# Kernel tuning notes

Hardware: AMD Instinct MI355X
Metric: run time of the kernel (lower is better)

Reference implementation:

```python
import jax, jax.numpy as jnp
import numpy as np

B, T, D, H = 4, 2048, 512, 8
SCALE = np.float32(1.0 / np.sqrt(D))  # 'vaswani' scale, tied scalar, non-trainable
MASK_BIAS = np.float32(1e9)           # TF dense_attention masking constant


def setup_inputs() -> dict:
    key = jax.random.key(0)
    ks = jax.random.split(key, 5)
    s = 0.02  # small init so softmax logits are well-scaled
    return {
        "query": jax.random.normal(ks[0], (B, T, D), jnp.float32),
        "value": jax.random.normal(ks[1], (B, T, D), jnp.float32),
        "Wq": jax.random.normal(ks[2], (D, D * H), jnp.float32) * s,
        "bq": jnp.zeros((D * H,), jnp.float32),
        "Wk": jax.random.normal(ks[3], (D, D * H), jnp.float32) * s,
        "bk": jnp.zeros((D * H,), jnp.float32),
        "Wv": jax.random.normal(ks[4], (D, D * H), jnp.float32) * s,
        "bv": jnp.zeros((D * H,), jnp.float32),
    }


def reference(query, value, Wq, bq, Wk, bk, Wv, bv):
    # Per-head Dense projections (linear activation, depth=1): [B,T,D] -> [B,T,H*D]
    # split(axis=-1) into H heads + concat(axis=0) == reshape to [B,T,H,D]
    # (head h occupies contiguous slice [h*D:(h+1)*D] of the last axis)
    q = (query @ Wq + bq).reshape(B, T, H, D)
    k = (value @ Wk + bk).reshape(B, T, H, D)  # key defaults to value
    v = (value @ Wv + bv).reshape(B, T, H, D)
    # multiplicative scores: matmul(scale*q, k^T) -> [B,H,Tq,Tv]
    scores = jnp.einsum('bqhd,bkhd->bhqk', SCALE * q, k)
    # causal mask applied TF-style: scores -= 1e9 * (~mask)
    causal = jnp.tril(jnp.ones((T, T), bool))
    scores = jnp.where(causal, scores, scores - MASK_BIAS)
    attn = jax.nn.softmax(scores, axis=-1)          # [B,H,Tq,Tv]
    out = jnp.einsum('bhqk,bkhd->bqhd', attn, v)    # [B,Tq,H,D]
    # heads_output_mode='cat': concat heads back on feature axis
    return out.reshape(B, T, H * D)
```

## Files before the change

### kernel.cpp

```cpp
#include <hip/hip_runtime.h>
#include <stdint.h>

#define Bsz 4
#define Tsz 2048
#define Dsz 512
#define Hsz 8
#define HDsz 4096
#define Msz 8192
#define SCALE 0.044194173824159216f

typedef __attribute__((ext_vector_type(8))) short bf16x8;
typedef __attribute__((ext_vector_type(4))) float f32x4;
typedef __attribute__((ext_vector_type(4))) short s16x4;

static __device__ __forceinline__ short f2bf(float x) {
    uint32_t b = __float_as_uint(x);
    b += 0x7fff + ((b >> 16) & 1);
    return (short)(b >> 16);
}

__global__ __launch_bounds__(256) void xcast_kernel(
    const float* __restrict__ Xq, const float* __restrict__ Xv,
    short* __restrict__ Oq, short* __restrict__ Ov)
{
    int idx = blockIdx.x * 256 + threadIdx.x;
    const float* src = (idx < 1048576) ? Xq : Xv;
    short* dst = (idx < 1048576) ? Oq : Ov;
    int i = (idx < 1048576) ? idx : idx - 1048576;
    float4 v = *(const float4*)&src[(size_t)i * 4];
    s16x4 o;
    o.x = f2bf(v.x); o.y = f2bf(v.y); o.z = f2bf(v.z); o.w = f2bf(v.w);
    *(s16x4*)&dst[(size_t)i * 4] = o;
}

__global__ __launch_bounds__(256) void wtrans_kernel(
    const float* __restrict__ Wq, const float* __restrict__ Wk,
    const float* __restrict__ Wv, short* __restrict__ WtAll)
{
    const float* W = (blockIdx.z == 0) ? Wq : (blockIdx.z == 1) ? Wk : Wv;
    short* Wt = WtAll + (size_t)blockIdx.z * (size_t)HDsz * Dsz;
    __shared__ float tile[32][33];
    int tx = threadIdx.x, ty = threadIdx.y;
    int k0 = blockIdx.x * 32, n0 = blockIdx.y * 32;
    for (int i = 0; i < 4; i++)
        tile[ty + i * 8][tx] = W[(size_t)(k0 + ty + i * 8) * HDsz + n0 + tx];
    __syncthreads();
    for (int i = 0; i < 4; i++)
        Wt[(size_t)(n0 + ty + i * 8) * Dsz + k0 + tx] = f2bf(tile[tx][ty + i * 8]);
}

__global__ __launch_bounds__(256, 2) void proj_gemm_kernel(
    const short* __restrict__ Xqb, const short* __restrict__ Xvb,
    const short* __restrict__ WtAll, const float* __restrict__ bq,
    const float* __restrict__ bk, const float* __restrict__ bv,
    short* __restrict__ Qo, short* __restrict__ Ko, short* __restrict__ Vto)
{
    const int mode = blockIdx.z;
    const short* X = (mode == 0) ? Xqb : Xvb;
    const short* Wt = WtAll + (size_t)mode * (size_t)HDsz * Dsz;
    const float* bias = (mode == 0) ? bq : (mode == 1) ? bk : bv;
    const int m0 = blockIdx.x * 128, n0 = blockIdx.y * 128;

    __shared__ short sm[17408];

    const int tid = threadIdx.x;
    const int lane = tid & 63, wave = tid >> 6;
    const int quad = lane >> 4, l16 = lane & 15;
    const int wm = wave >> 1, wn = wave & 1;

    const int dmarow = lane >> 2;
    const int dmachunk = (lane & 3) ^ ((lane >> 3) & 3);
    const int rdsw = (quad ^ ((l16 >> 1) & 3)) * 8;

    f32x4 acc[4][4];
    for (int i = 0; i < 4; i++)
        for (int j = 0; j < 4; j++)
            acc[i][j] = f32x4{0.f, 0.f, 0.f, 0.f};

#define STAGE(ksv, bufsel) do {                                                  \
        const int _ks = (ksv);                                                   \
        short* _A = sm + (bufsel) * 4096;                                        \
        short* _B = sm + 8192 + (bufsel) * 4096;                                 \
        for (int s = 0; s < 2; s++) {                                            \
            int c = wave * 2 + s;                                                \
            int row = c * 16 + dmarow;                                           \
            const short* ga = X + (size_t)(m0 + row) * Dsz + _ks + dmachunk * 8; \
            __builtin_amdgcn_global_load_lds(                                    \
                (const __attribute__((address_space(1))) void*)ga,               \
                (__attribute__((address_space(3))) void*)&_A[c * 512], 16, 0, 0);\
            const short* gb = Wt + (size_t)(n0 + row) * Dsz + _ks + dmachunk * 8;\
            __builtin_amdgcn_global_load_lds(                                    \
                (const __attribute__((address_space(1))) void*)gb,               \
                (__attribute__((address_space(3))) void*)&_B[c * 512], 16, 0, 0);\
        }                                                                        \
    } while (0)

    STAGE(0, 0);
    __syncthreads();

    for (int t = 0; t < 16; t++) {
        const int cur = t & 1;
        if (t < 15) STAGE((t + 1) * 32, cur ^ 1);
        const short* Ac = sm + cur * 4096;
        const short* Bc = sm + 8192 + cur * 4096;
        bf16x8 af[4], bfr[4];
        for (int i = 0; i < 4; i++)
            af[i] = *(const bf16x8*)&Ac[(wm * 64 + i * 16 + l16) * 32 + rdsw];
        for (int j = 0; j < 4; j++)
            bfr[j] = *(const bf16x8*)&Bc[(wn * 64 + j * 16 + l16) * 32 + rdsw];
        for (int i = 0; i < 4; i++)
            for (int j = 0; j < 4; j++)
                acc[i][j] = __builtin_amdgcn_mfma_f32_16x16x32_bf16(
                    af[i], bfr[j], acc[i][j], 0, 0, 0);
        __syncthreads();
    }
#undef STAGE

    const int b = m0 >> 11, t0 = m0 & 2047;
    const int h = n0 >> 9, d0 = n0 & 511;
    const float scv = (mode == 0) ? SCALE : 1.0f;

    if (mode == 2) {
        for (int i = 0; i < 4; i++)
            for (int j = 0; j < 4; j++) {
                int c = wn * 64 + j * 16 + l16;
                float bb = bias[n0 + c];
                int rb = wm * 64 + i * 16 + quad * 4;
                for (int r = 0; r < 4; r++)
                    sm[c * 136 + rb + r] = f2bf(acc[i][j][r] + bb);
            }
    } else {
        for (int i = 0; i < 4; i++)
            for (int j = 0; j < 4; j++) {
                int c = wn * 64 + j * 16 + l16;
                float bb = bias[n0 + c];
                int rb = wm * 64 + i * 16 + quad * 4;
                for (int r = 0; r < 4; r++)
                    sm[(rb + r) * 136 + c] = f2bf((acc[i][j][r] + bb) * scv);
            }
    }
    __syncthreads();

    if (mode == 2) {
        size_t base = ((size_t)(b * Hsz + h) * Dsz + d0) * Tsz + t0;
        for (int k = 0; k < 8; k++) {
            int cid = k * 256 + tid;
            int c = cid >> 4, r8 = (cid & 15) * 8;
            *(bf16x8*)&Vto[base + (size_t)c * Tsz + r8] =
                *(const bf16x8*)&sm[c * 136 + r8];
        }
    } else {
        short* O = (mode == 0) ? Qo : Ko;
        size_t base = ((size_t)(b * Hsz + h) * Tsz + t0) * Dsz + d0;
        for (int k = 0; k < 8; k++) {
            int cid = k * 256 + tid;
            int r = cid >> 4, c8 = (cid & 15) * 8;
            *(bf16x8*)&O[base + (size_t)r * Dsz + c8] =
                *(const bf16x8*)&sm[r * 136 + c8];
        }
    }
}

__global__ __launch_bounds__(512, 2) void attn_kernel(
    const short* __restrict__ Q, const short* __restrict__ K,
    const short* __restrict__ Vt, float* __restrict__ out)
{
    extern __shared__ short smem[];

    const int bid = blockIdx.x;
    const int qt = 15 - (bid >> 5);
    const int bh = bid & 31;
    const int q0 = qt * 128;
    const short* Qb = Q + (size_t)bh * Tsz * Dsz;
    const short* Kb = K + (size_t)bh * Tsz * Dsz;
    const short* Vb = Vt + (size_t)bh * Dsz * Tsz;

    const int tid = threadIdx.x;
    const int lane = tid & 63, wave = tid >> 6;
    const int quad = lane >> 4, l16 = lane & 15;
    const int qw = q0 + wave * 16;
    short* Pw = smem + 74240 + wave * (16 * 40);
    const int vrow = tid >> 2, vch = tid & 3;

    bf16x8 qf[16];
    for (int ks = 0; ks < 16; ks++)
        qf[ks] = *(const bf16x8*)&Qb[(size_t)(qw + l16) * Dsz + ks * 32 + quad * 8];

    f32x4 acc[32];
    for (int dt = 0; dt < 32; dt++) acc[dt] = f32x4{0.f, 0.f, 0.f, 0.f};
    float lacc[4] = {0.f, 0.f, 0.f, 0.f};

    {
        short* Ks0 = smem;
        short* Vs0 = smem + 33280;
        for (int i = 0; i < 4; i++) {
            int r = wave * 4 + i;
            const short* gp = Kb + (size_t)r * Dsz + lane * 8;
            __builtin_amdgcn_global_load_lds(
                (const __attribute__((address_space(1))) void*)gp,
                (__attribute__((address_space(3))) void*)&Ks0[r * 520], 16, 0, 0);
        }
        for (int p = 0; p < 4; p++) {
            int row = p * 128 + vrow;
            bf16x8 v = *(const bf16x8*)&Vb[(size_t)row * Tsz + vch * 8];
            *(bf16x8*)&Vs0[row * 40 + vch * 8] = v;
        }
    }
    __syncthreads();

    const int nkv = 4 * (qt + 1);
    for (int kt = 0; kt < nkv; kt++) {
        const int kv0 = kt * 32;
        short* Ksc = smem + (kt & 1) * 16640;
        short* Vsc = smem + 33280 + (kt & 1) * 20480;
        const bool pref = (kt + 1 < nkv);

        bf16x8 vreg[4];
        if (pref) {
            const int kvn = kv0 + 32;
            short* Ksn = smem + ((kt + 1) & 1) * 16640;
            for (int i = 0; i < 4; i++) {
                int r = wave * 4 + i;
                const short* gp = Kb + (size_t)(kvn + r) * Dsz + lane * 8;
                __builtin_amdgcn_global_load_lds(
                    (const __attribute__((address_space(1))) void*)gp,
                    (__attribute__((address_space(3))) void*)&Ksn[r * 520], 16, 0, 0);
            }
            for (int p = 0; p < 4; p++) {
                int row = p * 128 + vrow;
                vreg[p] = *(const bf16x8*)&Vb[(size_t)row * Tsz + kvn + vch * 8];
            }
        }

        if (kv0 <= qw + 15) {
            f32x4 s0 = f32x4{0.f, 0.f, 0.f, 0.f}, s1 = f32x4{0.f, 0.f, 0.f, 0.f};
            for (int ks = 0; ks < 16; ks++) {
                bf16x8 b0 = *(const bf16x8*)&Ksc[l16 * 520 + ks * 32 + quad * 8];
                bf16x8 b1 = *(const bf16x8*)&Ksc[(16 + l16) * 520 + ks * 32 + quad * 8];
                s0 = __builtin_amdgcn_mfma_f32_16x16x32_bf16(qf[ks], b0, s0, 0, 0, 0);
                s1 = __builtin_amdgcn_mfma_f32_16x16x32_bf16(qf[ks], b1, s1, 0, 0, 0);
            }
            bool full = (kv0 + 31 <= qw);
            for (int r = 0; r < 4; r++) {
                int rowg = qw + quad * 4 + r;
                float p0 = __expf(fminf(s0[r], 40.f));
                float p1 = __expf(fminf(s1[r], 40.f));
                if (!full) {
                    if (kv0 + l16 > rowg) p0 = 0.f;
                    if (kv0 + 16 + l16 > rowg) p1 = 0.f;
                }
                lacc[r] += p0 + p1;
                Pw[(quad * 4 + r) * 40 + l16] = f2bf(p0);
                Pw[(quad * 4 + r) * 40 + 16 + l16] = f2bf(p1);
            }
            bf16x8 pa = *(const bf16x8*)&Pw[l16 * 40 + quad * 8];
            for (int dt = 0; dt < 32; dt++) {
                bf16x8 vb = *(const bf16x8*)&Vsc[(dt * 16 + l16) * 40 + quad * 8];
                acc[dt] = __builtin_amdgcn_mfma_f32_16x16x32_bf16(pa, vb, acc[dt], 0, 0, 0);
            }
        }

        if (pref) {
            short* Vsn = smem + 33280 + ((kt + 1) & 1) * 20480;
            for (int p = 0; p < 4; p++) {
                int row = p * 128 + vrow;
                *(bf16x8*)&Vsn[row * 40 + vch * 8] = vreg[p];
            }
        }
        __syncthreads();
    }

    const int b = bh >> 3, h = bh & 7;
    float inv[4];
    for (int r = 0; r < 4; r++) {
        float l = lacc[r];
        l += __shfl_xor(l, 1);
        l += __shfl_xor(l, 2);
        l += __shfl_xor(l, 4);
        l += __shfl_xor(l, 8);
        inv[r] = 1.0f / l;
    }
    for (int dt = 0; dt < 32; dt++) {
        for (int r = 0; r < 4; r++) {
            int t = qw + quad * 4 + r;
            out[(size_t)(b * Tsz + t) * HDsz + h * Dsz + dt * 16 + l16] =
                acc[dt][r] * inv[r];
        }
    }
}

extern "C" void kernel_launch(void* const* d_in, const int* in_sizes, int n_in,
                              void* d_out, int out_size, void* d_ws, size_t ws_size,
                              hipStream_t stream) {
    const float* query = (const float*)d_in[0];
    const float* value = (const float*)d_in[1];
    const float* Wq = (const float*)d_in[2];
    const float* bq = (const float*)d_in[3];
    const float* Wk = (const float*)d_in[4];
    const float* bk = (const float*)d_in[5];
    const float* Wv = (const float*)d_in[6];
    const float* bv = (const float*)d_in[7];
    float* out = (float*)d_out;

    char* ws = (char*)d_ws;
    short* Wt  = (short*)ws;
    short* Xqb = (short*)(ws + 12582912);
    short* Xvb = (short*)(ws + 20971520);
    short* Qb  = (short*)(ws + 29360128);
    short* Kb  = (short*)(ws + 96468992);
    short* Vtb = (short*)(ws + 163577856);

    (void)hipFuncSetAttribute((const void*)attn_kernel,
                        hipFuncAttributeMaxDynamicSharedMemorySize, 158720);

    xcast_kernel<<<8192, 256, 0, stream>>>(query, value, Xqb, Xvb);
    wtrans_kernel<<<dim3(16, 128, 3), dim3(32, 8), 0, stream>>>(Wq, Wk, Wv, Wt);
    proj_gemm_kernel<<<dim3(64, 32, 3), 256, 0, stream>>>(
        Xqb, Xvb, Wt, bq, bk, bv, Qb, Kb, Vtb);
    attn_kernel<<<dim3(512), dim3(512), 158720, stream>>>(Qb, Kb, Vtb, out);
}
```

Before: 538.7 us.

## Repartition PV product so each wave owns a D-slice across all query rows

The P@V stage is restructured. Each wave used to multiply its own 16 query rows against all 512 V columns, reading the whole V tile from LDS. Now every wave writes its P tile to shared memory, a barrier is added, and each wave keeps a 64-column slice of V in registers while looping over all 8 waves' P tiles. P tiles that are fully masked are skipped. This cuts LDS reads of V, at the cost of an extra __syncthreads per KV tile and a shared-memory pass to gather the row sums for the epilogue. The projection GEMM's launch-bounds occupancy hint is also raised from 2 to 3.

```diff
diff --git a/kernel.cpp b/kernel.cpp
--- a/kernel.cpp
+++ b/kernel.cpp
@@ -49,7 +49,7 @@
         Wt[(size_t)(n0 + ty + i * 8) * Dsz + k0 + tx] = f2bf(tile[tx][ty + i * 8]);
 }
 
-__global__ __launch_bounds__(256, 2) void proj_gemm_kernel(
+__global__ __launch_bounds__(256, 3) void proj_gemm_kernel(
     const short* __restrict__ Xqb, const short* __restrict__ Xvb,
     const short* __restrict__ WtAll, const float* __restrict__ bq,
     const float* __restrict__ bk, const float* __restrict__ bv,
@@ -179,7 +179,7 @@
     const int lane = tid & 63, wave = tid >> 6;
     const int quad = lane >> 4, l16 = lane & 15;
     const int qw = q0 + wave * 16;
-    short* Pw = smem + 74240 + wave * (16 * 40);
+    short* Pw = smem + 74240 + wave * 640;
     const int vrow = tid >> 2, vch = tid & 3;
 
     bf16x8 qf[16];
@@ -187,7 +187,7 @@
         qf[ks] = *(const bf16x8*)&Qb[(size_t)(qw + l16) * Dsz + ks * 32 + quad * 8];
 
     f32x4 acc[32];
-    for (int dt = 0; dt < 32; dt++) acc[dt] = f32x4{0.f, 0.f, 0.f, 0.f};
+    for (int i = 0; i < 32; i++) acc[i] = f32x4{0.f, 0.f, 0.f, 0.f};
     float lacc[4] = {0.f, 0.f, 0.f, 0.f};
 
     {
@@ -253,10 +253,20 @@
                 Pw[(quad * 4 + r) * 40 + l16] = f2bf(p0);
                 Pw[(quad * 4 + r) * 40 + 16 + l16] = f2bf(p1);
             }
-            bf16x8 pa = *(const bf16x8*)&Pw[l16 * 40 + quad * 8];
-            for (int dt = 0; dt < 32; dt++) {
-                bf16x8 vb = *(const bf16x8*)&Vsc[(dt * 16 + l16) * 40 + quad * 8];
-                acc[dt] = __builtin_amdgcn_mfma_f32_16x16x32_bf16(pa, vb, acc[dt], 0, 0, 0);
+        }
+        __syncthreads();
+
+        {
+            bf16x8 vb[4];
+            for (int df = 0; df < 4; df++)
+                vb[df] = *(const bf16x8*)&Vsc[(wave * 64 + df * 16 + l16) * 40 + quad * 8];
+            for (int rf = 0; rf < 8; rf++) {
+                if (kv0 <= q0 + rf * 16 + 15) {
+                    bf16x8 pa = *(const bf16x8*)&smem[74240 + rf * 640 + l16 * 40 + quad * 8];
+                    for (int df = 0; df < 4; df++)
+                        acc[rf * 4 + df] = __builtin_amdgcn_mfma_f32_16x16x32_bf16(
+                            pa, vb[df], acc[rf * 4 + df], 0, 0, 0);
+                }
             }
         }
 
@@ -270,21 +280,25 @@
         __syncthreads();
     }
 
-    const int b = bh >> 3, h = bh & 7;
-    float inv[4];
+    float* lsh = (float*)(smem + 74240);
     for (int r = 0; r < 4; r++) {
         float l = lacc[r];
         l += __shfl_xor(l, 1);
         l += __shfl_xor(l, 2);
         l += __shfl_xor(l, 4);
         l += __shfl_xor(l, 8);
-        inv[r] = 1.0f / l;
-    }
-    for (int dt = 0; dt < 32; dt++) {
+        if (l16 == 0) lsh[wave * 16 + quad * 4 + r] = l;
+    }
+    __syncthreads();
+
+    const int b = bh >> 3, h = bh & 7;
+    for (int rf = 0; rf < 8; rf++) {
         for (int r = 0; r < 4; r++) {
-            int t = qw + quad * 4 + r;
-            out[(size_t)(b * Tsz + t) * HDsz + h * Dsz + dt * 16 + l16] =
-                acc[dt][r] * inv[r];
+            float invl = 1.0f / lsh[rf * 16 + quad * 4 + r];
+            int t = q0 + rf * 16 + quad * 4 + r;
+            float* op = &out[(size_t)(b * Tsz + t) * HDsz + h * Dsz + wave * 64 + l16];
+            for (int df = 0; df < 4; df++)
+                op[df * 16] = acc[rf * 4 + df][r] * invl;
         }
     }
 }
```

Result: no change. 547.1 us (+1.6%).

## Restructure attention into paired causal row blocks with register-loaded V fragments

Applied to the files above, without the earlier changes.

Each attention block now handles two 64-row query strips, one from the start and one from the end of the sequence, so every block does a balanced amount of causal work. PV is split so each wave owns a 128-column slice of D for all four row fragments, and V is read straight from global memory into registers instead of being staged in LDS. This frees shared memory, which allows four resident blocks per CU (proj_gemm is also raised to three). The cost is an extra barrier per KV tile, V fetched from global or cache by every wave without LDS sharing, and more register pressure under the tighter launch bounds, which could cause spills.

```diff
diff --git a/kernel.cpp b/kernel.cpp
--- a/kernel.cpp
+++ b/kernel.cpp
@@ -49,7 +49,7 @@
         Wt[(size_t)(n0 + ty + i * 8) * Dsz + k0 + tx] = f2bf(tile[tx][ty + i * 8]);
 }
 
-__global__ __launch_bounds__(256, 2) void proj_gemm_kernel(
+__global__ __launch_bounds__(256, 3) void proj_gemm_kernel(
     const short* __restrict__ Xqb, const short* __restrict__ Xvb,
     const short* __restrict__ WtAll, const float* __restrict__ bq,
     const float* __restrict__ bk, const float* __restrict__ bv,
@@ -161,16 +161,15 @@
     }
 }
 
-__global__ __launch_bounds__(512, 2) void attn_kernel(
+__global__ __launch_bounds__(512, 4) void attn_kernel(
     const short* __restrict__ Q, const short* __restrict__ K,
     const short* __restrict__ Vt, float* __restrict__ out)
 {
     extern __shared__ short smem[];
 
     const int bid = blockIdx.x;
-    const int qt = 15 - (bid >> 5);
+    const int ib = bid >> 5;
     const int bh = bid & 31;
-    const int q0 = qt * 128;
     const short* Qb = Q + (size_t)bh * Tsz * Dsz;
     const short* Kb = K + (size_t)bh * Tsz * Dsz;
     const short* Vb = Vt + (size_t)bh * Dsz * Tsz;
@@ -178,68 +177,66 @@
     const int tid = threadIdx.x;
     const int lane = tid & 63, wave = tid >> 6;
     const int quad = lane >> 4, l16 = lane & 15;
-    const int qw = q0 + wave * 16;
-    short* Pw = smem + 74240 + wave * (16 * 40);
-    const int vrow = tid >> 2, vch = tid & 3;
+    const int g = wave >> 2;
+    const int ws = wave & 3;
+    const int sr = (g == 0) ? ib * 64 : (31 - ib) * 64;
+    const int qw = sr + ws * 16;
+    short* Pw = smem + 33280 + wave * 640;
 
     bf16x8 qf[16];
     for (int ks = 0; ks < 16; ks++)
         qf[ks] = *(const bf16x8*)&Qb[(size_t)(qw + l16) * Dsz + ks * 32 + quad * 8];
 
     f32x4 acc[32];
-    for (int dt = 0; dt < 32; dt++) acc[dt] = f32x4{0.f, 0.f, 0.f, 0.f};
+    for (int i = 0; i < 32; i++) acc[i] = f32x4{0.f, 0.f, 0.f, 0.f};
     float lacc[4] = {0.f, 0.f, 0.f, 0.f};
 
-    {
-        short* Ks0 = smem;
-        short* Vs0 = smem + 33280;
-        for (int i = 0; i < 4; i++) {
-            int r = wave * 4 + i;
-            const short* gp = Kb + (size_t)r * Dsz + lane * 8;
-            __builtin_amdgcn_global_load_lds(
-                (const __attribute__((address_space(1))) void*)gp,
-                (__attribute__((address_space(3))) void*)&Ks0[r * 520], 16, 0, 0);
-        }
-        for (int p = 0; p < 4; p++) {
-            int row = p * 128 + vrow;
-            bf16x8 v = *(const bf16x8*)&Vb[(size_t)row * Tsz + vch * 8];
-            *(bf16x8*)&Vs0[row * 40 + vch * 8] = v;
-        }
-    }
-    __syncthreads();
-
-    const int nkv = 4 * (qt + 1);
+    for (int i = 0; i < 4; i++) {
+        int r = wave * 4 + i;
+        const short* gp = Kb + (size_t)r * Dsz + lane * 8;
+        __builtin_amdgcn_global_load_lds(
+            (const __attribute__((address_space(1))) void*)gp,
+            (__attribute__((address_space(3))) void*)&smem[r * 520], 16, 0, 0);
+    }
+    __syncthreads();
+
+    const int nkv = 2 * (32 - ib);
     for (int kt = 0; kt < nkv; kt++) {
         const int kv0 = kt * 32;
         short* Ksc = smem + (kt & 1) * 16640;
-        short* Vsc = smem + 33280 + (kt & 1) * 20480;
-        const bool pref = (kt + 1 < nkv);
-
-        bf16x8 vreg[4];
-        if (pref) {
-            const int kvn = kv0 + 32;
+
+        if (kt + 1 < nkv) {
             short* Ksn = smem + ((kt + 1) & 1) * 16640;
             for (int i = 0; i < 4; i++) {
                 int r = wave * 4 + i;
-                const short* gp = Kb + (size_t)(kvn + r) * Dsz + lane * 8;
+                const short* gp = Kb + (size_t)(kv0 + 32 + r) * Dsz + lane * 8;
                 __builtin_amdgcn_global_load_lds(
                     (const __attribute__((address_space(1))) void*)gp,
                     (__attribute__((address_space(3))) void*)&Ksn[r * 520], 16, 0, 0);
             }
-            for (int p = 0; p < 4; p++) {
-                int row = p * 128 + vrow;
-                vreg[p] = *(const bf16x8*)&Vb[(size_t)row * Tsz + kvn + vch * 8];
-            }
-        }
-
-        if (kv0 <= qw + 15) {
-            f32x4 s0 = f32x4{0.f, 0.f, 0.f, 0.f}, s1 = f32x4{0.f, 0.f, 0.f, 0.f};
+        }
+
+        const bool qact = (kv0 <= qw + 15);
+        const bool pvact = (kv0 <= sr + 63);
+
+        f32x4 s0 = f32x4{0.f, 0.f, 0.f, 0.f}, s1 = f32x4{0.f, 0.f, 0.f, 0.f};
+        if (qact) {
             for (int ks = 0; ks < 16; ks++) {
                 bf16x8 b0 = *(const bf16x8*)&Ksc[l16 * 520 + ks * 32 + quad * 8];
                 bf16x8 b1 = *(const bf16x8*)&Ksc[(16 + l16) * 520 + ks * 32 + quad * 8];
                 s0 = __builtin_amdgcn_mfma_f32_16x16x32_bf16(qf[ks], b0, s0, 0, 0, 0);
                 s1 = __builtin_amdgcn_mfma_f32_16x16x32_bf16(qf[ks], b1, s1, 0, 0, 0);
             }
+        }
+
+        bf16x8 vb[8];
+        if (pvact) {
+            for (int df = 0; df < 8; df++)
+                vb[df] = *(const bf16x8*)
+                    &Vb[(size_t)(ws * 128 + df * 16 + l16) * Tsz + kv0 + quad * 8];
+        }
+
+        if (qact) {
             bool full = (kv0 + 31 <= qw);
             for (int r = 0; r < 4; r++) {
                 int rowg = qw + quad * 4 + r;
@@ -253,38 +250,43 @@
                 Pw[(quad * 4 + r) * 40 + l16] = f2bf(p0);
                 Pw[(quad * 4 + r) * 40 + 16 + l16] = f2bf(p1);
             }
-            bf16x8 pa = *(const bf16x8*)&Pw[l16 * 40 + quad * 8];
-            for (int dt = 0; dt < 32; dt++) {
-                bf16x8 vb = *(const bf16x8*)&Vsc[(dt * 16 + l16) * 40 + quad * 8];
-                acc[dt] = __builtin_amdgcn_mfma_f32_16x16x32_bf16(pa, vb, acc[dt], 0, 0, 0);
-            }
-        }
-
-        if (pref) {
-            short* Vsn = smem + 33280 + ((kt + 1) & 1) * 20480;
-            for (int p = 0; p < 4; p++) {
-                int row = p * 128 + vrow;
-                *(bf16x8*)&Vsn[row * 40 + vch * 8] = vreg[p];
-            }
         }
         __syncthreads();
-    }
-
-    const int b = bh >> 3, h = bh & 7;
-    float inv[4];
+
+        if (pvact) {
+            for (int rf = 0; rf < 4; rf++) {
+                if (kv0 <= sr + rf * 16 + 15) {
+                    bf16x8 pa = *(const bf16x8*)
+                        &smem[33280 + (g * 4 + rf) * 640 + l16 * 40 + quad * 8];
+                    for (int df = 0; df < 8; df++)
+                        acc[rf * 8 + df] = __builtin_amdgcn_mfma_f32_16x16x32_bf16(
+                            pa, vb[df], acc[rf * 8 + df], 0, 0, 0);
+                }
+            }
+        }
+        __syncthreads();
+    }
+
+    float* lsh = (float*)(smem + 33280);
     for (int r = 0; r < 4; r++) {
         float l = lacc[r];
         l += __shfl_xor(l, 1);
         l += __shfl_xor(l, 2);
         l += __shfl_xor(l, 4);
         l += __shfl_xor(l, 8);
-        inv[r] = 1.0f / l;
-    }
-    for (int dt = 0; dt < 32; dt++) {
+        if (l16 == 0) lsh[wave * 16 + quad * 4 + r] = l;
+    }
+    __syncthreads();
+
+    const int b = bh >> 3, h = bh & 7;
+    for (int rf = 0; rf < 4; rf++) {
         for (int r = 0; r < 4; r++) {
-            int t = qw + quad * 4 + r;
-            out[(size_t)(b * Tsz + t) * HDsz + h * Dsz + dt * 16 + l16] =
-                acc[dt][r] * inv[r];
+            float invl = 1.0f / lsh[(g * 4 + rf) * 16 + quad * 4 + r];
+            int t = sr + rf * 16 + quad * 4 + r;
+            float* op = &out[(size_t)(b * Tsz + t) * HDsz + h * Dsz
+                             + ws * 128 + l16];
+            for (int df = 0; df < 8; df++)
+                op[df * 16] = acc[rf * 8 + df][r] * invl;
         }
     }
 }
@@ -311,11 +313,11 @@
     short* Vtb = (short*)(ws + 163577856);
 
     (void)hipFuncSetAttribute((const void*)attn_kernel,
-                        hipFuncAttributeMaxDynamicSharedMemorySize, 158720);
+                        hipFuncAttributeMaxDynamicSharedMemorySize, 76800);
 
     xcast_kernel<<<8192, 256, 0, stream>>>(query, value, Xqb, Xvb);
     wtrans_kernel<<<dim3(16, 128, 3), dim3(32, 8), 0, stream>>>(Wq, Wk, Wv, Wt);
     proj_gemm_kernel<<<dim3(64, 32, 3), 256, 0, stream>>>(
         Xqb, Xvb, Wt, bq, bk, bv, Qb, Kb, Vtb);
-    attn_kernel<<<dim3(512), dim3(512), 158720, stream>>>(Qb, Kb, Vtb, out);
-}
+    attn_kernel<<<dim3(512), dim3(512), 76800, stream>>>(Qb, Kb, Vtb, out);
+}
```

After: 1.895 ms. 3.52x slower.
